# Kernel optimization log

Measured on AMD Instinct MI355X. Metric: run time of the kernel, lower is better.

The kernel has to match this reference:

```python
import jax, jax.numpy as jnp
import numpy as np

N, E, D, H, C, L = 50000, 600000, 128, 128, 64, 3
LN_EPS = 1e-5


def setup_inputs() -> dict:
    key = jax.random.key(0)
    ks = jax.random.split(key, 6)
    x = jax.random.normal(ks[0], (N, D), jnp.float32)
    edge_index = jax.random.randint(ks[1], (2, E), 0, N, jnp.int32)
    Wg = jax.random.normal(ks[2], (L, D, H), jnp.float32) * (1.0 / np.sqrt(D))
    bg = jnp.zeros((L, H), jnp.float32)
    ln_g = jnp.ones((L, H), jnp.float32)
    ln_b = jnp.zeros((L, H), jnp.float32)
    mlp_W1 = jax.random.normal(ks[3], (D + L * H, H), jnp.float32) * (1.0 / np.sqrt(D + L * H))
    mlp_b1 = jnp.zeros((H,), jnp.float32)
    mlp_W2 = jax.random.normal(ks[4], (H, C), jnp.float32) * (1.0 / np.sqrt(H))
    mlp_b2 = jnp.zeros((C,), jnp.float32)
    return {"x": x, "edge_index": edge_index, "Wg": Wg, "bg": bg,
            "ln_g": ln_g, "ln_b": ln_b, "mlp_W1": mlp_W1, "mlp_b1": mlp_b1,
            "mlp_W2": mlp_W2, "mlp_b2": mlp_b2}


def _layer_norm(h, g, b):
    mu = jnp.mean(h, axis=-1, keepdims=True)
    var = jnp.mean((h - mu) ** 2, axis=-1, keepdims=True)
    return g * (h - mu) * jax.lax.rsqrt(var + LN_EPS) + b


def _gcn(h, W, b, src, dst, dinv):
    # GCNConv with added self-loops and symmetric normalization:
    # out = D^{-1/2} (A + I) D^{-1/2} (h W) + b
    hW = h @ W                                   # [N, H]
    coef = (dinv[src] * dinv[dst])[:, None]      # [E, 1]
    agg = jax.ops.segment_sum(hW[src] * coef, dst, num_segments=N)
    agg = agg + hW * (dinv * dinv)[:, None]      # self-loop term
    return agg + b


def reference(x, edge_index, Wg, bg, ln_g, ln_b, mlp_W1, mlp_b1, mlp_W2, mlp_b2):
    src, dst = edge_index[0], edge_index[1]
    # degree including self-loop
    deg = jnp.ones((N,), x.dtype).at[dst].add(1.0)
    dinv = jax.lax.rsqrt(deg)
    feats = [x]
    h = x
    for i in range(L):  # small fixed layer count
        h = _gcn(h, Wg[i], bg[i], src, dst, dinv)
        h = _layer_norm(h, ln_g[i], ln_b[i])
        h = jax.nn.relu(h)
        feats.append(h)
    xc = jnp.concatenate(feats, axis=1)          # [N, D + L*H]
    z = jax.nn.relu(xc @ mlp_W1 + mlp_b1)
    z = z @ mlp_W2 + mlp_b2
    return jax.nn.softmax(z, axis=1)
```

## Files before the change

### kernel.cpp

```cpp
#include <hip/hip_runtime.h>
#include <math.h>

#define D 128
#define HH 128
#define CC 64
#define NLAYERS 3
#define LN_EPS 1e-5f

typedef __attribute__((ext_vector_type(8))) short bf16x8;
typedef __attribute__((ext_vector_type(4))) float f32x4;
typedef unsigned short u16;
typedef unsigned int u32;

__device__ __forceinline__ u16 f2bf(float f) {
    u32 u = __float_as_uint(f);
    u32 r = u + 0x7FFFu + ((u >> 16) & 1u);
    return (u16)(r >> 16);
}
__device__ __forceinline__ float bf2f(u16 h) {
    return __uint_as_float(((u32)h) << 16);
}


__global__ void k_zero_cnt(int* __restrict__ cnt, int n) {
    int i = blockIdx.x * blockDim.x + threadIdx.x;
    if (i < n) cnt[i] = 0;
}

__global__ void k_count(const int* __restrict__ dst, int* __restrict__ cnt, int E) {
    int i = blockIdx.x * blockDim.x + threadIdx.x;
    if (i < E) atomicAdd(&cnt[dst[i]], 1);
}

__global__ void k_scan_a(const int* __restrict__ cnt, int* __restrict__ rowptr,
                         int* __restrict__ bsum, int N) {
    __shared__ int s[1024];
    int tid = threadIdx.x;
    int i = blockIdx.x * 1024 + tid;
    int v = (i < N) ? cnt[i] : 0;
    s[tid] = v;
    __syncthreads();
    for (int off = 1; off < 1024; off <<= 1) {
        int t = (tid >= off) ? s[tid - off] : 0;
        __syncthreads();
        s[tid] += t;
        __syncthreads();
    }
    if (i < N) rowptr[i] = s[tid] - v;
    if (tid == 1023) bsum[blockIdx.x] = s[tid];
}

__global__ void k_scan_b(int* __restrict__ bsum, int nb) {
    int t = threadIdx.x;
    int v = (t < nb) ? bsum[t] : 0;
    int incl = v;
    for (int off = 1; off < 64; off <<= 1) {
        int u = __shfl_up(incl, off, 64);
        if (t >= off) incl += u;
    }
    if (t < nb) bsum[t] = incl - v;
}

__global__ void k_scan_c(int* __restrict__ rowptr, const int* __restrict__ bsum,
                         const int* __restrict__ cnt, float* __restrict__ dinv,
                         int* __restrict__ cursor, int N, int E) {
    int i = blockIdx.x * blockDim.x + threadIdx.x;
    if (i < N) {
        int v = rowptr[i] + bsum[i >> 10];
        rowptr[i] = v;
        cursor[i] = v;
        dinv[i] = rsqrtf(1.0f + (float)cnt[i]);
    }
    if (i == 0) rowptr[N] = E;
}

__global__ void k_scatter(const int* __restrict__ src, const int* __restrict__ dst,
                          const float* __restrict__ dinv,
                          int* __restrict__ cursor, int2* __restrict__ ecol, int E) {
    int i = blockIdx.x * blockDim.x + threadIdx.x;
    if (i < E) {
        int s = src[i], d = dst[i];
        int p = atomicAdd(&cursor[d], 1);
        float c = dinv[s] * dinv[d];
        ecol[p] = make_int2(s, __float_as_int(c));
    }
}


__global__ void k_split_x(const float* __restrict__ x, u16* __restrict__ xh,
                          u16* __restrict__ xl, int total) {
    int i = blockIdx.x * blockDim.x + threadIdx.x;
    if (i >= total) return;
    int row = i >> 7, c = i & 127;
    float v = x[i];
    u16 h = f2bf(v);
    u16 l = f2bf(v - bf2f(h));
    xh[(size_t)row * 512 + c] = h;
    xl[(size_t)row * 128 + c] = l;
}

__global__ void k_tile_w(const float* __restrict__ W, u16* __restrict__ th,
                         u16* __restrict__ tl, int KN, int nshift) {
    int idx = blockIdx.x * blockDim.x + threadIdx.x;
    if (idx >= KN) return;
    int k = idx >> nshift, n = idx & ((1 << nshift) - 1);
    int kc = k >> 5, q = (k >> 3) & 3, j = k & 7;
    float v = W[idx];
    u16 h = f2bf(v);
    int o = (((kc * 4 + q) << nshift) + n) * 8 + j;
    th[o] = h;
    if (tl) tl[o] = f2bf(v - bf2f(h));
}

template <bool SPLIT2>
__global__ __launch_bounds__(256) void k_gemm_lf(
    const u16* __restrict__ Ahi, int strideA, int colOff,
    const u16* __restrict__ Alo, int strideAlo,
    const u16* __restrict__ Bt, u16* __restrict__ OUTb, int N)
{
    const int tid  = threadIdx.x;
    const int lane = tid & 63;
    const int wave = tid >> 6;
    const int wr   = wave & 1;
    const int wc   = wave >> 1;
    const int quad = lane >> 4;
    const int l15  = lane & 15;
    const int row0 = blockIdx.x * 64;

    const u16* pAh[2];
    const u16* pAl[2];
    #pragma unroll
    for (int i = 0; i < 2; ++i) {
        int r = row0 + wr * 32 + i * 16 + l15;
        if (r >= N) r = N - 1;
        pAh[i] = Ahi + (size_t)r * strideA + colOff + quad * 8;
        if (SPLIT2) pAl[i] = Alo + (size_t)r * strideAlo + quad * 8;
    }
    const u16* pB = Bt + ((size_t)quad * 128 + wc * 64 + l15) * 8;

    bf16x8 ah[4][2], al[4][2], bh[4][4];
    #pragma unroll
    for (int kc = 0; kc < 4; ++kc) {
        #pragma unroll
        for (int i = 0; i < 2; ++i) {
            ah[kc][i] = *(const bf16x8*)(pAh[i] + kc * 32);
            if (SPLIT2) al[kc][i] = *(const bf16x8*)(pAl[i] + kc * 32);
        }
        #pragma unroll
        for (int j = 0; j < 4; ++j)
            bh[kc][j] = *(const bf16x8*)(pB + (size_t)kc * 4096 + j * 128);
    }

    f32x4 acc[2][4];
    #pragma unroll
    for (int i = 0; i < 2; ++i)
        #pragma unroll
        for (int j = 0; j < 4; ++j)
            #pragma unroll
            for (int r = 0; r < 4; ++r) acc[i][j][r] = 0.f;

    #pragma unroll
    for (int kc = 0; kc < 4; ++kc)
        #pragma unroll
        for (int i = 0; i < 2; ++i)
            #pragma unroll
            for (int j = 0; j < 4; ++j) {
                acc[i][j] = __builtin_amdgcn_mfma_f32_16x16x32_bf16(ah[kc][i], bh[kc][j], acc[i][j], 0, 0, 0);
                if (SPLIT2)
                    acc[i][j] = __builtin_amdgcn_mfma_f32_16x16x32_bf16(al[kc][i], bh[kc][j], acc[i][j], 0, 0, 0);
            }

    #pragma unroll
    for (int i = 0; i < 2; ++i)
        #pragma unroll
        for (int j = 0; j < 4; ++j) {
            int col = wc * 64 + j * 16 + l15;
            #pragma unroll
            for (int r = 0; r < 4; ++r) {
                int grow = row0 + wr * 32 + i * 16 + quad * 4 + r;
                if (grow < N)
                    OUTb[(size_t)grow * 128 + col] = f2bf(acc[i][j][r]);
            }
        }
}

__global__ __launch_bounds__(256) void k_mlp_fused(
    const u16* __restrict__ xcH, const u16* __restrict__ xl,
    const u16* __restrict__ B1t, const float* __restrict__ b1,
    const u16* __restrict__ W2h, const u16* __restrict__ W2l,
    const float* __restrict__ b2, float* __restrict__ out, int N)
{
    __shared__ u16 sZh[64 * 128];
    __shared__ u16 sZl[64 * 128];

    const int tid  = threadIdx.x;
    const int lane = tid & 63;
    const int wave = tid >> 6;
    const int wr   = wave & 1;
    const int wc   = wave >> 1;
    const int quad = lane >> 4;
    const int l15  = lane & 15;
    const int row0 = blockIdx.x * 64;

    const u16* pAh[2];
    const u16* pAl[2];
    #pragma unroll
    for (int f = 0; f < 2; ++f) {
        int r = row0 + wr * 32 + f * 16 + l15;
        if (r >= N) r = N - 1;
        pAh[f] = xcH + (size_t)r * 512 + quad * 8;
        pAl[f] = xl  + (size_t)r * 128 + quad * 8;
    }
    const u16* pB = B1t + ((size_t)quad * 128 + wc * 64 + l15) * 8;

    f32x4 acc[2][4];
    #pragma unroll
    for (int f = 0; f < 2; ++f)
        #pragma unroll
        for (int j = 0; j < 4; ++j)
            #pragma unroll
            for (int r = 0; r < 4; ++r) acc[f][j][r] = 0.f;

    bf16x8 abuf[4][2], bbuf[4][4];
    #define LOADI(i, s)                                                          \
        {                                                                        \
            const int bk = ((i) < 16) ? (i) : ((i) - 16);                        \
            _Pragma("unroll")                                                    \
            for (int f = 0; f < 2; ++f)                                          \
                abuf[s][f] = ((i) < 16)                                          \
                    ? *(const bf16x8*)(pAh[f] + (i) * 32)                        \
                    : *(const bf16x8*)(pAl[f] + ((i) - 16) * 32);                \
            _Pragma("unroll")                                                    \
            for (int j = 0; j < 4; ++j)                                          \
                bbuf[s][j] = *(const bf16x8*)(pB + (size_t)bk * 4096 + j * 128); \
        }
    LOADI(0, 0)
    LOADI(1, 1)
    LOADI(2, 2)
    #pragma unroll
    for (int i = 0; i < 20; ++i) {
        if (i + 3 < 20) {
            const int s = (i + 3) & 3;
            LOADI(i + 3, s)
        }
        const int u = i & 3;
        #pragma unroll
        for (int f = 0; f < 2; ++f)
            #pragma unroll
            for (int j = 0; j < 4; ++j)
                acc[f][j] = __builtin_amdgcn_mfma_f32_16x16x32_bf16(abuf[u][f], bbuf[u][j], acc[f][j], 0, 0, 0);
    }
    #undef LOADI

    #pragma unroll
    for (int jt = 0; jt < 4; ++jt) {
        int col = wc * 64 + jt * 16 + l15;
        float bv = b1[col];
        int qq = col >> 3, jj = col & 7;
        #pragma unroll
        for (int f = 0; f < 2; ++f) {
            #pragma unroll
            for (int rr = 0; rr < 4; ++rr) {
                int r = wr * 32 + f * 16 + quad * 4 + rr;
                float v = fmaxf(acc[f][jt][rr] + bv, 0.f);
                u16 h = f2bf(v);
                sZh[(qq * 64 + r) * 8 + jj] = h;
                sZl[(qq * 64 + r) * 8 + jj] = f2bf(v - bf2f(h));
            }
        }
    }
    __syncthreads();

    f32x4 oacc[4];
    #pragma unroll
    for (int j = 0; j < 4; ++j)
        #pragma unroll
        for (int r = 0; r < 4; ++r) oacc[j][r] = 0.f;

    #pragma unroll
    for (int kc = 0; kc < 4; ++kc) {
        int qq = kc * 4 + quad;
        bf16x8 zh = *(const bf16x8*)&sZh[(qq * 64 + wave * 16 + l15) * 8];
        bf16x8 zl = *(const bf16x8*)&sZl[(qq * 64 + wave * 16 + l15) * 8];
        #pragma unroll
        for (int jt = 0; jt < 4; ++jt) {
            int n = jt * 16 + l15;
            bf16x8 wh = *(const bf16x8*)&W2h[(qq * 64 + n) * 8];
            bf16x8 wl = *(const bf16x8*)&W2l[(qq * 64 + n) * 8];
            oacc[jt] = __builtin_amdgcn_mfma_f32_16x16x32_bf16(zh, wh, oacc[jt], 0, 0, 0);
            oacc[jt] = __builtin_amdgcn_mfma_f32_16x16x32_bf16(zh, wl, oacc[jt], 0, 0, 0);
            oacc[jt] = __builtin_amdgcn_mfma_f32_16x16x32_bf16(zl, wh, oacc[jt], 0, 0, 0);
        }
    }

    #pragma unroll
    for (int jt = 0; jt < 4; ++jt) {
        float bv = b2[jt * 16 + l15];
        #pragma unroll
        for (int r = 0; r < 4; ++r) oacc[jt][r] += bv;
    }
    #pragma unroll
    for (int r = 0; r < 4; ++r) {
        float m = fmaxf(fmaxf(oacc[0][r], oacc[1][r]), fmaxf(oacc[2][r], oacc[3][r]));
        #pragma unroll
        for (int mask = 8; mask; mask >>= 1) m = fmaxf(m, __shfl_xor(m, mask, 64));
        float p0 = __expf(oacc[0][r] - m);
        float p1 = __expf(oacc[1][r] - m);
        float p2 = __expf(oacc[2][r] - m);
        float p3 = __expf(oacc[3][r] - m);
        float s = p0 + p1 + p2 + p3;
        #pragma unroll
        for (int mask = 8; mask; mask >>= 1) s += __shfl_xor(s, mask, 64);
        float inv = 1.0f / s;
        int grow = row0 + wave * 16 + quad * 4 + r;
        if (grow < N) {
            float* o = out + (size_t)grow * CC + l15;
            o[0]  = p0 * inv;
            o[16] = p1 * inv;
            o[32] = p2 * inv;
            o[48] = p3 * inv;
        }
    }
}

__global__ __launch_bounds__(256, 8) void k_agg_ln(
    const u16* __restrict__ hWb,
    const int* __restrict__ rowptr, const int2* __restrict__ ecol,
    const float* __restrict__ dinv,
    const float* __restrict__ bg, const float* __restrict__ g,
    const float* __restrict__ b,
    u16* __restrict__ outHi, int N)
{
    const int lane = threadIdx.x & 63;
    const int f0 = lane * 2;

    const float bgx = bg[f0], bgy = bg[f0 + 1];
    const float gx  = g[f0],  gy  = g[f0 + 1];
    const float bx  = b[f0],  by  = b[f0 + 1];

    const int nwaves = gridDim.x * 4;
    for (int wid = blockIdx.x * 4 + (threadIdx.x >> 6); wid < N; wid += nwaves) {
        float di = dinv[wid];
        float sc = di * di;

        u32 hv = *(const u32*)(hWb + (size_t)wid * HH + f0);
        float ax  = bf2f((u16)hv) * sc;
        float ay  = bf2f((u16)(hv >> 16)) * sc;
        float ax1 = 0.f, ay1 = 0.f, ax2 = 0.f, ay2 = 0.f, ax3 = 0.f, ay3 = 0.f;

        int e0 = rowptr[wid];
        int e1 = rowptr[wid + 1];
        int e = e0;
        for (; e + 8 <= e1; e += 8) {
            int2 p[8];
            u32  v[8];
            #pragma unroll
            for (int t = 0; t < 8; ++t) p[t] = ecol[e + t];
            #pragma unroll
            for (int t = 0; t < 8; ++t)
                v[t] = *(const u32*)(hWb + (size_t)p[t].x * HH + f0);
            #pragma unroll
            for (int t = 0; t < 8; ++t) {
                float c = __int_as_float(p[t].y);
                float vx = bf2f((u16)v[t]) * c;
                float vy = bf2f((u16)(v[t] >> 16)) * c;
                switch (t & 3) {
                    case 0: ax  += vx; ay  += vy; break;
                    case 1: ax1 += vx; ay1 += vy; break;
                    case 2: ax2 += vx; ay2 += vy; break;
                    default: ax3 += vx; ay3 += vy; break;
                }
            }
        }
        for (; e + 4 <= e1; e += 4) {
            int2 p0 = ecol[e];
            int2 p1 = ecol[e + 1];
            int2 p2 = ecol[e + 2];
            int2 p3 = ecol[e + 3];
            u32 v0 = *(const u32*)(hWb + (size_t)p0.x * HH + f0);
            u32 v1 = *(const u32*)(hWb + (size_t)p1.x * HH + f0);
            u32 v2 = *(const u32*)(hWb + (size_t)p2.x * HH + f0);
            u32 v3 = *(const u32*)(hWb + (size_t)p3.x * HH + f0);
            ax  += bf2f((u16)v0) * __int_as_float(p0.y);  ay  += bf2f((u16)(v0 >> 16)) * __int_as_float(p0.y);
            ax1 += bf2f((u16)v1) * __int_as_float(p1.y);  ay1 += bf2f((u16)(v1 >> 16)) * __int_as_float(p1.y);
            ax2 += bf2f((u16)v2) * __int_as_float(p2.y);  ay2 += bf2f((u16)(v2 >> 16)) * __int_as_float(p2.y);
            ax3 += bf2f((u16)v3) * __int_as_float(p3.y);  ay3 += bf2f((u16)(v3 >> 16)) * __int_as_float(p3.y);
        }
        for (; e < e1; ++e) {
            int2 p = ecol[e];
            u32 v = *(const u32*)(hWb + (size_t)p.x * HH + f0);
            float c = __int_as_float(p.y);
            ax += bf2f((u16)v) * c;
            ay += bf2f((u16)(v >> 16)) * c;
        }
        ax += ax1 + ax2 + ax3;
        ay += ay1 + ay2 + ay3;
        ax += bgx;
        ay += bgy;

        float ssum = ax + ay;
        #pragma unroll
        for (int off = 32; off; off >>= 1) ssum += __shfl_xor(ssum, off, 64);
        float mu = ssum * (1.0f / 128.0f);
        float dx = ax - mu, dy = ay - mu;
        float vsum = dx * dx + dy * dy;
        #pragma unroll
        for (int off = 32; off; off >>= 1) vsum += __shfl_xor(vsum, off, 64);
        float rstd = rsqrtf(vsum * (1.0f / 128.0f) + LN_EPS);

        float ox = fmaxf(gx * dx * rstd + bx, 0.f);
        float oy = fmaxf(gy * dy * rstd + by, 0.f);

        *(u32*)&outHi[(size_t)wid * 512 + f0] = (u32)f2bf(ox) | ((u32)f2bf(oy) << 16);
    }
}

extern "C" void kernel_launch(void* const* d_in, const int* in_sizes, int n_in,
                              void* d_out, int out_size, void* d_ws, size_t ws_size,
                              hipStream_t stream) {
    const float* x   = (const float*)d_in[0];
    const int*   ei  = (const int*)  d_in[1];
    const float* Wg  = (const float*)d_in[2];
    const float* bg  = (const float*)d_in[3];
    const float* lng = (const float*)d_in[4];
    const float* lnb = (const float*)d_in[5];
    const float* W1  = (const float*)d_in[6];
    const float* b1  = (const float*)d_in[7];
    const float* W2  = (const float*)d_in[8];
    const float* b2  = (const float*)d_in[9];
    float* out = (float*)d_out;

    const int N = in_sizes[0] / D;
    const int E = in_sizes[1] / 2;
    const int* srcp = ei;
    const int* dstp = ei + E;

    char* ws = (char*)d_ws;
    size_t off = 0;
    auto alloc = [&](size_t bytes) -> void* {
        void* p = ws + off;
        off += (bytes + 511) & ~(size_t)511;
        return p;
    };
    int*   cnt    = (int*)  alloc((size_t)N * 4);
    int*   rowptr = (int*)  alloc((size_t)(N + 1) * 4);
    int*   cursor = (int*)  alloc((size_t)N * 4);
    int*   bsum   = (int*)  alloc(64 * 4);
    int2*  ecol   = (int2*) alloc((size_t)E * 8);
    float* dinv   = (float*)alloc((size_t)N * 4);
    u16*   hWb    = (u16*)  alloc((size_t)N * HH * 2);
    u16*   xcH    = (u16*)  alloc((size_t)N * 512 * 2);
    u16*   xl     = (u16*)  alloc((size_t)N * 128 * 2);
    u16*   WgtH   = (u16*)  alloc((size_t)NLAYERS * D * HH * 2);
    u16*   W1tH   = (u16*)  alloc((size_t)(D + NLAYERS * HH) * HH * 2);
    u16*   W2tH   = (u16*)  alloc((size_t)HH * CC * 2);
    u16*   W2tL   = (u16*)  alloc((size_t)HH * CC * 2);

    const int B = 256;
    const int gN = (N + B - 1) / B;
    const int gE = (E + B - 1) / B;
    const int nsb = (N + 1023) / 1024;

    k_zero_cnt<<<gN, B, 0, stream>>>(cnt, N);
    k_count<<<gE, B, 0, stream>>>(dstp, cnt, E);
    k_scan_a<<<nsb, 1024, 0, stream>>>(cnt, rowptr, bsum, N);
    k_scan_b<<<1, 64, 0, stream>>>(bsum, nsb);
    k_scan_c<<<gN, B, 0, stream>>>(rowptr, bsum, cnt, dinv, cursor, N, E);
    k_scatter<<<gE, B, 0, stream>>>(srcp, dstp, dinv, cursor, ecol, E);

    k_split_x<<<(N * D + B - 1) / B, B, 0, stream>>>(x, xcH, xl, N * D);
    for (int l = 0; l < NLAYERS; ++l)
        k_tile_w<<<(D * HH + B - 1) / B, B, 0, stream>>>(Wg + (size_t)l * D * HH,
                                                         WgtH + (size_t)l * D * HH,
                                                         nullptr, D * HH, 7);
    k_tile_w<<<((D + NLAYERS * HH) * HH + B - 1) / B, B, 0, stream>>>(W1, W1tH, nullptr,
                                                                      (D + NLAYERS * HH) * HH, 7);
    k_tile_w<<<(HH * CC + B - 1) / B, B, 0, stream>>>(W2, W2tH, W2tL, HH * CC, 6);

    const int gemmBlocks = (N + 63) / 64;
    const int aggBlocks  = 2048;

    for (int l = 0; l < NLAYERS; ++l) {
        if (l == 0)
            k_gemm_lf<true><<<gemmBlocks, B, 0, stream>>>(xcH, 512, 0, xl, 128,
                                                          WgtH, hWb, N);
        else
            k_gemm_lf<false><<<gemmBlocks, B, 0, stream>>>(xcH, 512, l * HH, nullptr, 0,
                                                           WgtH + (size_t)l * D * HH, hWb, N);
        k_agg_ln<<<aggBlocks, B, 0, stream>>>(hWb, rowptr, ecol, dinv,
                                              bg + (size_t)l * HH,
                                              lng + (size_t)l * HH,
                                              lnb + (size_t)l * HH,
                                              xcH + (size_t)(l + 1) * HH, N);
    }

    k_mlp_fused<<<gemmBlocks, B, 0, stream>>>(xcH, xl, W1tH, b1,
                                              W2tH, W2tL, b2, out, N);
}
```

Measured before the change: 346.8 us.

## Split MLP K-dimension across wave pairs with 32-row tiles and LDS reduction

The fused MLP kernel now processes 32 rows per block instead of 64. The two wave pairs each take half of the 20 K-steps of the first GEMM, and their partial sums are combined through a shared-memory float buffer before bias, ReLU and the second GEMM. This doubles the block count and shortens each wave's serial MFMA chain, which should give more parallelism and latency hiding. The cost is an extra LDS reduction, an extra barrier, and half the waves sitting idle during the second GEMM and softmax. The three per-layer weight tiling launches are also merged into one.

```diff
diff --git a/kernel.cpp b/kernel.cpp
--- a/kernel.cpp
+++ b/kernel.cpp
@@ -190,23 +190,24 @@
     const u16* __restrict__ W2h, const u16* __restrict__ W2l,
     const float* __restrict__ b2, float* __restrict__ out, int N)
 {
-    __shared__ u16 sZh[64 * 128];
-    __shared__ u16 sZl[64 * 128];
+    __shared__ float sAcc[32 * 132];
+    __shared__ u16 sZh[32 * 128];
+    __shared__ u16 sZl[32 * 128];
 
     const int tid  = threadIdx.x;
     const int lane = tid & 63;
     const int wave = tid >> 6;
-    const int wr   = wave & 1;
-    const int wc   = wave >> 1;
+    const int wc   = wave & 1;
+    const int kg   = wave >> 1;
     const int quad = lane >> 4;
     const int l15  = lane & 15;
-    const int row0 = blockIdx.x * 64;
+    const int row0 = blockIdx.x * 32;
 
     const u16* pAh[2];
     const u16* pAl[2];
     #pragma unroll
     for (int f = 0; f < 2; ++f) {
-        int r = row0 + wr * 32 + f * 16 + l15;
+        int r = row0 + f * 16 + l15;
         if (r >= N) r = N - 1;
         pAh[f] = xcH + (size_t)r * 512 + quad * 8;
         pAl[f] = xl  + (size_t)r * 128 + quad * 8;
@@ -221,29 +222,31 @@
             #pragma unroll
             for (int r = 0; r < 4; ++r) acc[f][j][r] = 0.f;
 
-    bf16x8 abuf[4][2], bbuf[4][4];
-    #define LOADI(i, s)                                                          \
+    bf16x8 abuf[3][2], bbuf[3][4];
+    #define LOADI(t, s)                                                          \
         {                                                                        \
-            const int bk = ((i) < 16) ? (i) : ((i) - 16);                        \
+            const int g = kg * 10 + (t);                                         \
+            const int hi = (g < 16);                                             \
+            const int bk = hi ? g : g - 16;                                      \
             _Pragma("unroll")                                                    \
-            for (int f = 0; f < 2; ++f)                                          \
-                abuf[s][f] = ((i) < 16)                                          \
-                    ? *(const bf16x8*)(pAh[f] + (i) * 32)                        \
-                    : *(const bf16x8*)(pAl[f] + ((i) - 16) * 32);                \
+            for (int f = 0; f < 2; ++f) {                                        \
+                const u16* pa = hi ? (pAh[f] + g * 32)                           \
+                                   : (pAl[f] + (g - 16) * 32);                   \
+                abuf[s][f] = *(const bf16x8*)pa;                                 \
+            }                                                                    \
             _Pragma("unroll")                                                    \
             for (int j = 0; j < 4; ++j)                                          \
                 bbuf[s][j] = *(const bf16x8*)(pB + (size_t)bk * 4096 + j * 128); \
         }
     LOADI(0, 0)
     LOADI(1, 1)
-    LOADI(2, 2)
-    #pragma unroll
-    for (int i = 0; i < 20; ++i) {
-        if (i + 3 < 20) {
-            const int s = (i + 3) & 3;
-            LOADI(i + 3, s)
-        }
-        const int u = i & 3;
+    #pragma unroll
+    for (int t = 0; t < 10; ++t) {
+        if (t + 2 < 10) {
+            const int s = (t + 2) % 3;
+            LOADI(t + 2, s)
+        }
+        const int u = t % 3;
         #pragma unroll
         for (int f = 0; f < 2; ++f)
             #pragma unroll
@@ -252,73 +255,91 @@
     }
     #undef LOADI
 
-    #pragma unroll
-    for (int jt = 0; jt < 4; ++jt) {
-        int col = wc * 64 + jt * 16 + l15;
-        float bv = b1[col];
-        int qq = col >> 3, jj = col & 7;
-        #pragma unroll
-        for (int f = 0; f < 2; ++f) {
-            #pragma unroll
-            for (int rr = 0; rr < 4; ++rr) {
-                int r = wr * 32 + f * 16 + quad * 4 + rr;
-                float v = fmaxf(acc[f][jt][rr] + bv, 0.f);
-                u16 h = f2bf(v);
-                sZh[(qq * 64 + r) * 8 + jj] = h;
-                sZl[(qq * 64 + r) * 8 + jj] = f2bf(v - bf2f(h));
-            }
-        }
+    if (kg == 1) {
+        #pragma unroll
+        for (int f = 0; f < 2; ++f)
+            #pragma unroll
+            for (int jt = 0; jt < 4; ++jt) {
+                int col = wc * 64 + jt * 16 + l15;
+                #pragma unroll
+                for (int r = 0; r < 4; ++r) {
+                    int row = f * 16 + quad * 4 + r;
+                    sAcc[row * 132 + col] = acc[f][jt][r];
+                }
+            }
     }
     __syncthreads();
-
-    f32x4 oacc[4];
-    #pragma unroll
-    for (int j = 0; j < 4; ++j)
-        #pragma unroll
-        for (int r = 0; r < 4; ++r) oacc[j][r] = 0.f;
-
-    #pragma unroll
-    for (int kc = 0; kc < 4; ++kc) {
-        int qq = kc * 4 + quad;
-        bf16x8 zh = *(const bf16x8*)&sZh[(qq * 64 + wave * 16 + l15) * 8];
-        bf16x8 zl = *(const bf16x8*)&sZl[(qq * 64 + wave * 16 + l15) * 8];
+    if (kg == 0) {
         #pragma unroll
         for (int jt = 0; jt < 4; ++jt) {
-            int n = jt * 16 + l15;
-            bf16x8 wh = *(const bf16x8*)&W2h[(qq * 64 + n) * 8];
-            bf16x8 wl = *(const bf16x8*)&W2l[(qq * 64 + n) * 8];
-            oacc[jt] = __builtin_amdgcn_mfma_f32_16x16x32_bf16(zh, wh, oacc[jt], 0, 0, 0);
-            oacc[jt] = __builtin_amdgcn_mfma_f32_16x16x32_bf16(zh, wl, oacc[jt], 0, 0, 0);
-            oacc[jt] = __builtin_amdgcn_mfma_f32_16x16x32_bf16(zl, wh, oacc[jt], 0, 0, 0);
-        }
-    }
-
-    #pragma unroll
-    for (int jt = 0; jt < 4; ++jt) {
-        float bv = b2[jt * 16 + l15];
-        #pragma unroll
-        for (int r = 0; r < 4; ++r) oacc[jt][r] += bv;
-    }
-    #pragma unroll
-    for (int r = 0; r < 4; ++r) {
-        float m = fmaxf(fmaxf(oacc[0][r], oacc[1][r]), fmaxf(oacc[2][r], oacc[3][r]));
-        #pragma unroll
-        for (int mask = 8; mask; mask >>= 1) m = fmaxf(m, __shfl_xor(m, mask, 64));
-        float p0 = __expf(oacc[0][r] - m);
-        float p1 = __expf(oacc[1][r] - m);
-        float p2 = __expf(oacc[2][r] - m);
-        float p3 = __expf(oacc[3][r] - m);
-        float s = p0 + p1 + p2 + p3;
-        #pragma unroll
-        for (int mask = 8; mask; mask >>= 1) s += __shfl_xor(s, mask, 64);
-        float inv = 1.0f / s;
-        int grow = row0 + wave * 16 + quad * 4 + r;
-        if (grow < N) {
-            float* o = out + (size_t)grow * CC + l15;
-            o[0]  = p0 * inv;
-            o[16] = p1 * inv;
-            o[32] = p2 * inv;
-            o[48] = p3 * inv;
+            int col = wc * 64 + jt * 16 + l15;
+            float bv = b1[col];
+            int qq = col >> 3, jj = col & 7;
+            #pragma unroll
+            for (int f = 0; f < 2; ++f) {
+                #pragma unroll
+                for (int rr = 0; rr < 4; ++rr) {
+                    int row = f * 16 + quad * 4 + rr;
+                    float v = fmaxf(acc[f][jt][rr] + sAcc[row * 132 + col] + bv, 0.f);
+                    u16 h = f2bf(v);
+                    sZh[(qq * 32 + row) * 8 + jj] = h;
+                    sZl[(qq * 32 + row) * 8 + jj] = f2bf(v - bf2f(h));
+                }
+            }
+        }
+    }
+    __syncthreads();
+
+    if (kg == 0) {
+        f32x4 oacc[4];
+        #pragma unroll
+        for (int j = 0; j < 4; ++j)
+            #pragma unroll
+            for (int r = 0; r < 4; ++r) oacc[j][r] = 0.f;
+
+        #pragma unroll
+        for (int kc = 0; kc < 4; ++kc) {
+            int qq = kc * 4 + quad;
+            bf16x8 zh = *(const bf16x8*)&sZh[(qq * 32 + wc * 16 + l15) * 8];
+            bf16x8 zl = *(const bf16x8*)&sZl[(qq * 32 + wc * 16 + l15) * 8];
+            #pragma unroll
+            for (int jt = 0; jt < 4; ++jt) {
+                int n = jt * 16 + l15;
+                bf16x8 wh = *(const bf16x8*)&W2h[(qq * 64 + n) * 8];
+                bf16x8 wl = *(const bf16x8*)&W2l[(qq * 64 + n) * 8];
+                oacc[jt] = __builtin_amdgcn_mfma_f32_16x16x32_bf16(zh, wh, oacc[jt], 0, 0, 0);
+                oacc[jt] = __builtin_amdgcn_mfma_f32_16x16x32_bf16(zh, wl, oacc[jt], 0, 0, 0);
+                oacc[jt] = __builtin_amdgcn_mfma_f32_16x16x32_bf16(zl, wh, oacc[jt], 0, 0, 0);
+            }
+        }
+
+        #pragma unroll
+        for (int jt = 0; jt < 4; ++jt) {
+            float bv = b2[jt * 16 + l15];
+            #pragma unroll
+            for (int r = 0; r < 4; ++r) oacc[jt][r] += bv;
+        }
+        #pragma unroll
+        for (int r = 0; r < 4; ++r) {
+            float m = fmaxf(fmaxf(oacc[0][r], oacc[1][r]), fmaxf(oacc[2][r], oacc[3][r]));
+            #pragma unroll
+            for (int mask = 8; mask; mask >>= 1) m = fmaxf(m, __shfl_xor(m, mask, 64));
+            float p0 = __expf(oacc[0][r] - m);
+            float p1 = __expf(oacc[1][r] - m);
+            float p2 = __expf(oacc[2][r] - m);
+            float p3 = __expf(oacc[3][r] - m);
+            float s = p0 + p1 + p2 + p3;
+            #pragma unroll
+            for (int mask = 8; mask; mask >>= 1) s += __shfl_xor(s, mask, 64);
+            float inv = 1.0f / s;
+            int grow = row0 + wc * 16 + quad * 4 + r;
+            if (grow < N) {
+                float* o = out + (size_t)grow * CC + l15;
+                o[0]  = p0 * inv;
+                o[16] = p1 * inv;
+                o[32] = p2 * inv;
+                o[48] = p3 * inv;
+            }
         }
     }
 }
@@ -469,15 +490,14 @@
     k_scatter<<<gE, B, 0, stream>>>(srcp, dstp, dinv, cursor, ecol, E);
 
     k_split_x<<<(N * D + B - 1) / B, B, 0, stream>>>(x, xcH, xl, N * D);
-    for (int l = 0; l < NLAYERS; ++l)
-        k_tile_w<<<(D * HH + B - 1) / B, B, 0, stream>>>(Wg + (size_t)l * D * HH,
-                                                         WgtH + (size_t)l * D * HH,
-                                                         nullptr, D * HH, 7);
+    k_tile_w<<<(NLAYERS * D * HH + B - 1) / B, B, 0, stream>>>(Wg, WgtH, nullptr,
+                                                               NLAYERS * D * HH, 7);
     k_tile_w<<<((D + NLAYERS * HH) * HH + B - 1) / B, B, 0, stream>>>(W1, W1tH, nullptr,
                                                                       (D + NLAYERS * HH) * HH, 7);
     k_tile_w<<<(HH * CC + B - 1) / B, B, 0, stream>>>(W2, W2tH, W2tL, HH * CC, 6);
 
     const int gemmBlocks = (N + 63) / 64;
+    const int mlpBlocks  = (N + 31) / 32;
     const int aggBlocks  = 2048;
 
     for (int l = 0; l < NLAYERS; ++l) {
@@ -494,6 +514,6 @@
                                               xcH + (size_t)(l + 1) * HH, N);
     }
 
-    k_mlp_fused<<<gemmBlocks, B, 0, stream>>>(xcH, xl, W1tH, b1,
-                                              W2tH, W2tL, b2, out, N);
-}
+    k_mlp_fused<<<mlpBlocks, B, 0, stream>>>(xcH, xl, W1tH, b1,
+                                             W2tH, W2tL, b2, out, N);
+}
```

Result: faster. 333.7 us (-3.8%).
